# Kernel optimization log

Measured on AMD Instinct MI355X. Metric: run time of the kernel, lower is better.

Reference implementation:

```python
import jax, jax.numpy as jnp
import numpy as np

E = 256  # embedding_dim
H = 256  # hidden_dim
B = 65536


def setup_inputs() -> dict:
    key = jax.random.key(0)
    ks = jax.random.split(key, 15)
    inp = {
        "x": jax.random.normal(ks[0], (B, E), dtype=jnp.float32),
        "c": jax.random.normal(ks[1], (B, H), dtype=jnp.float32),
        "h": jax.random.normal(ks[2], (B, H), dtype=jnp.float32),
    }
    names = ["W_i", "U_i", "b_i", "W_f", "U_f", "b_f", "W_c", "U_c", "b_c", "W_o", "U_o", "b_o"]
    shapes = [(E, H), (H, H), (H,)] * 4
    for n, s, k in zip(names, shapes, ks[3:]):
        inp[n] = jax.random.normal(k, s, dtype=jnp.float32)
    return inp


def reference(x, c, h, W_i, U_i, b_i, W_f, U_f, b_f, W_c, U_c, b_c, W_o, U_o, b_o):
    # Batch the four input/hidden projections into two GEMMs, then fuse gates.
    W = jnp.concatenate([W_f, W_i, W_o, W_c], axis=1)  # [E, 4H]
    U = jnp.concatenate([U_f, U_i, U_o, U_c], axis=1)  # [H, 4H]
    b = jnp.concatenate([b_f, b_i, b_o, b_c], axis=0)  # [4H]
    z = x @ W + h @ U + b                               # [B, 4H]
    zf, zi, zo, zg = jnp.split(z, 4, axis=1)
    f = jax.nn.sigmoid(zf)
    i = jax.nn.sigmoid(zi)
    o = jax.nn.sigmoid(zo)
    g = jnp.tanh(zg)
    c_new = c * f + g * i
    h_new = o * jnp.tanh(c_new)
    return (c_new, h_new)
```

## Files before the change

kernel.cpp:

```cpp
#include <hip/hip_runtime.h>
#include <hip/hip_fp16.h>

typedef _Float16 half8 __attribute__((ext_vector_type(8)));
typedef _Float16 half4 __attribute__((ext_vector_type(4)));
typedef float f32x4 __attribute__((ext_vector_type(4)));

#define BHSZ 16777216
#define SLOT_BYTES 32768
#define B_OFF 16384
#define SBAR() __builtin_amdgcn_s_barrier()
#define WAITL() asm volatile("s_waitcnt lgkmcnt(0)" ::: "memory")

__device__ __forceinline__ void gload16(const void* g, const void* lds) {
  __builtin_amdgcn_global_load_lds((const __attribute__((address_space(1))) void*)g,
                                   (__attribute__((address_space(3))) void*)lds,
                                   16, 0, 0);
}

__device__ __forceinline__ float fast_sigmoid(float z) {
  float e = __builtin_amdgcn_exp2f(-z * 1.4426950408889634f);
  return __builtin_amdgcn_rcpf(1.0f + e);
}

__device__ __forceinline__ float fast_tanh(float z) {
  float a = __builtin_fabsf(z);
  float e = __builtin_amdgcn_exp2f(a * 2.8853900817779268f);
  float t = 1.0f - 2.0f * __builtin_amdgcn_rcpf(1.0f + e);
  return z < 0.0f ? -t : t;
}

__global__ __launch_bounds__(256) void pack_b(
    const float* __restrict__ Wf, const float* __restrict__ Uf,
    const float* __restrict__ Wi, const float* __restrict__ Ui,
    const float* __restrict__ Wo, const float* __restrict__ Uo,
    const float* __restrict__ Wc, const float* __restrict__ Uc,
    _Float16* __restrict__ Bp) {
  int idx = blockIdx.x * 256 + threadIdx.x;
  int k = idx & 511;
  int Np = idx >> 9;
  int g = (Np >> 4) & 3;
  int cl = ((Np >> 6) << 4) | (Np & 15);
  const float* W;
  const float* U;
  switch (g) {
    case 0: W = Wf; U = Uf; break;
    case 1: W = Wi; U = Ui; break;
    case 2: W = Wo; U = Uo; break;
    default: W = Wc; U = Uc; break;
  }
  float v = (k < 256) ? W[k * 256 + cl] : U[(k - 256) * 256 + cl];
  Bp[idx] = (_Float16)v;
}

__global__ __launch_bounds__(512, 2) void lstm_fused(
    const float* __restrict__ x, const float* __restrict__ h,
    const _Float16* __restrict__ Bp, const float* __restrict__ cin,
    const float* __restrict__ bf_, const float* __restrict__ bi_,
    const float* __restrict__ bo_, const float* __restrict__ bc_,
    float* __restrict__ out) {
  extern __shared__ __align__(16) char smem[];

  int tid = threadIdx.x;
  int w = tid >> 6, l = tid & 63;
  int l15 = l & 15, lg = l >> 4;
  int wr = w >> 2, wcn = w & 3;

  int bid = blockIdx.x;
  int wg = (bid & 7) * 128 + (bid >> 3);
  int bm = wg >> 2, bn = wg & 3;

  int aRowLo = tid >> 3;
  int aKpos = (tid & 7) * 4;
  int aWoff[4];
#pragma unroll
  for (int p = 0; p < 4; ++p) {
    int row = p * 64 + aRowLo;
    int rp = row >> 1;
    int c = ((((row & 1) << 2) | (aKpos >> 3)) ^ (rp & 7));
    aWoff[p] = rp * 128 + (c << 4) + ((tid & 1) << 3);
  }

  int fB[2];
#pragma unroll
  for (int p = 0; p < 2; ++p) {
    int d = p * 512 + tid;
    int rp = d >> 3, s8 = d & 7;
    int i8 = s8 ^ (rp & 7);
    int r = rp * 2 + (i8 >> 2), cb = i8 & 3;
    fB[p] = (bn * 256 + r) * 512 + (cb << 3);
  }
  int ldsB[2];
#pragma unroll
  for (int p = 0; p < 2; ++p) ldsB[p] = B_OFF + (p * 512 + w * 64) * 16;

  int offA[8], offB[4];
#pragma unroll
  for (int mf = 0; mf < 8; ++mf) {
    int r = wr * 128 + mf * 16 + l15;
    int rp = r >> 1;
    offA[mf] = rp * 128 + (((((r & 1) << 2) | lg) ^ (rp & 7)) << 4);
  }
#pragma unroll
  for (int nf = 0; nf < 4; ++nf) {
    int r = wcn * 64 + nf * 16 + l15;
    int rp = r >> 1;
    offB[nf] = B_OFF + rp * 128 + (((((r & 1) << 2) | lg) ^ (rp & 7)) << 4);
  }

  f32x4 acc[8][4];
#pragma unroll
  for (int a2 = 0; a2 < 8; ++a2)
#pragma unroll
    for (int b2 = 0; b2 < 4; ++b2)
      acc[a2][b2] = (f32x4){0.f, 0.f, 0.f, 0.f};

  f32x4 aReg[4];

  auto issueA = [&](int t) {
    const float* src = (t < 8) ? x : h;
    int kb = (t & 7) * 32;
#pragma unroll
    for (int p = 0; p < 4; ++p) {
      long row = (long)(bm * 256 + p * 64 + aRowLo);
      aReg[p] = *reinterpret_cast<const f32x4*>(src + row * 256 + kb + aKpos);
    }
  };
  auto issueB = [&](int t) {
    char* db = smem + (t % 3) * SLOT_BYTES;
#pragma unroll
    for (int p = 0; p < 2; ++p)
      gload16(Bp + fB[p] + t * 32, db + ldsB[p]);
  };
  auto writeA = [&](int t) {
    char* db = smem + (t % 3) * SLOT_BYTES;
#pragma unroll
    for (int p = 0; p < 4; ++p) {
      half4 o;
      o[0] = (_Float16)aReg[p][0]; o[1] = (_Float16)aReg[p][1];
      o[2] = (_Float16)aReg[p][2]; o[3] = (_Float16)aReg[p][3];
      *reinterpret_cast<half4*>(db + aWoff[p]) = o;
    }
  };

  issueB(0);
  issueA(0);
  asm volatile("s_waitcnt vmcnt(0)" ::: "memory");
  writeA(0);
  issueA(1);
  issueB(1);

#pragma unroll
  for (int j = 0; j < 16; ++j) {
    if (j == 15)
      asm volatile("s_waitcnt vmcnt(0)" ::: "memory");
    else
      asm volatile("s_waitcnt vmcnt(2)" ::: "memory");
    WAITL();
    SBAR();
    if (j <= 14) writeA(j + 1);
    if (j <= 13) issueA(j + 2);
    if (j <= 13) issueB(j + 2);

    const char* sb = smem + (j % 3) * SLOT_BYTES;
    half8 bv[4];
#pragma unroll
    for (int nf = 0; nf < 4; ++nf)
      bv[nf] = *reinterpret_cast<const half8*>(sb + offB[nf]);
#pragma unroll
    for (int bat = 0; bat < 2; ++bat) {
      half8 av[4];
#pragma unroll
      for (int q = 0; q < 4; ++q)
        av[q] = *reinterpret_cast<const half8*>(sb + offA[bat * 4 + q]);
      __builtin_amdgcn_s_setprio(1);
#pragma unroll
      for (int q = 0; q < 4; ++q)
#pragma unroll
        for (int nf = 0; nf < 4; ++nf)
          acc[bat * 4 + q][nf] = __builtin_amdgcn_mfma_f32_16x16x32_f16(
              av[q], bv[nf], acc[bat * 4 + q][nf], 0, 0, 0);
      __builtin_amdgcn_s_setprio(0);
    }
  }

  int col = (bn * 4 + wcn) * 16 + l15;
  float vbf = bf_[col], vbi = bi_[col], vbo = bo_[col], vbc = bc_[col];
#pragma unroll
  for (int mf = 0; mf < 8; ++mf) {
#pragma unroll
    for (int r = 0; r < 4; ++r) {
      long row = (long)(bm * 256 + wr * 128 + mf * 16 + lg * 4 + r);
      float zf = acc[mf][0][r] + vbf;
      float zi = acc[mf][1][r] + vbi;
      float zo = acc[mf][2][r] + vbo;
      float zg = acc[mf][3][r] + vbc;
      float fg = fast_sigmoid(zf);
      float ig = fast_sigmoid(zi);
      float og = fast_sigmoid(zo);
      float gg = fast_tanh(zg);
      float cv = cin[row * 256 + col];
      float cn = cv * fg + gg * ig;
      float hn = og * fast_tanh(cn);
      out[row * 256 + col] = cn;
      out[BHSZ + row * 256 + col] = hn;
    }
  }
}

extern "C" void kernel_launch(void* const* d_in, const int* in_sizes, int n_in,
                              void* d_out, int out_size, void* d_ws, size_t ws_size,
                              hipStream_t stream) {
  const float* x  = (const float*)d_in[0];
  const float* c  = (const float*)d_in[1];
  const float* h  = (const float*)d_in[2];
  const float* Wi = (const float*)d_in[3];
  const float* Ui = (const float*)d_in[4];
  const float* bi = (const float*)d_in[5];
  const float* Wf = (const float*)d_in[6];
  const float* Uf = (const float*)d_in[7];
  const float* bf = (const float*)d_in[8];
  const float* Wc = (const float*)d_in[9];
  const float* Uc = (const float*)d_in[10];
  const float* bc = (const float*)d_in[11];
  const float* Wo = (const float*)d_in[12];
  const float* Uo = (const float*)d_in[13];
  const float* bo = (const float*)d_in[14];

  _Float16* Bp = (_Float16*)d_ws;

  pack_b<<<2048, 256, 0, stream>>>(Wf, Uf, Wi, Ui, Wo, Uo, Wc, Uc, Bp);
  lstm_fused<<<1024, 512, 3 * SLOT_BYTES, stream>>>(x, h, Bp, c, bf, bi, bo,
                                                    bc, (float*)d_out);
}
```

Measured before the change: 149.1 us.

## Halve M-tile to 128 rows with 4 waves, double-buffer A, triple-buffer B

The workgroup tile drops from 256x256 to 128x256, run by 4 waves instead of 8 and launched as 2048 blocks. A is now double-buffered separately from triple-buffered B in a static 64KB LDS, and A stores are widened to 16-byte half8 writes. Sched barriers are added to pin the instruction order. Each B tile is now loaded by twice as many blocks, which raises L2 traffic for B, and with 64KB of LDS per block occupancy may fall.

```diff
diff --git a/kernel.cpp b/kernel.cpp
--- a/kernel.cpp
+++ b/kernel.cpp
@@ -2,13 +2,14 @@
 #include <hip/hip_fp16.h>
 
 typedef _Float16 half8 __attribute__((ext_vector_type(8)));
-typedef _Float16 half4 __attribute__((ext_vector_type(4)));
 typedef float f32x4 __attribute__((ext_vector_type(4)));
 
 #define BHSZ 16777216
-#define SLOT_BYTES 32768
-#define B_OFF 16384
+#define A_SLOT 8192
+#define B_SLOT 16384
+#define B_BASE 16384
 #define SBAR() __builtin_amdgcn_s_barrier()
+#define SCHEDB() __builtin_amdgcn_sched_barrier(0)
 #define WAITL() asm volatile("s_waitcnt lgkmcnt(0)" ::: "memory")
 
 __device__ __forceinline__ void gload16(const void* g, const void* lds) {
@@ -52,59 +53,56 @@
   Bp[idx] = (_Float16)v;
 }
 
-__global__ __launch_bounds__(512, 2) void lstm_fused(
+__global__ __launch_bounds__(256, 2) void lstm_fused(
     const float* __restrict__ x, const float* __restrict__ h,
     const _Float16* __restrict__ Bp, const float* __restrict__ cin,
     const float* __restrict__ bf_, const float* __restrict__ bi_,
     const float* __restrict__ bo_, const float* __restrict__ bc_,
     float* __restrict__ out) {
-  extern __shared__ __align__(16) char smem[];
+  __shared__ __align__(16) char smem[65536];
 
   int tid = threadIdx.x;
   int w = tid >> 6, l = tid & 63;
   int l15 = l & 15, lg = l >> 4;
-  int wr = w >> 2, wcn = w & 3;
 
   int bid = blockIdx.x;
-  int wg = (bid & 7) * 128 + (bid >> 3);
+  int wg = (bid & 7) * 256 + (bid >> 3);
   int bm = wg >> 2, bn = wg & 3;
 
-  int aRowLo = tid >> 3;
-  int aKpos = (tid & 7) * 4;
-  int aWoff[4];
+  int arow = tid >> 1;
+  int akq = (tid & 1) << 4;
+  const float* aSrcX = x + (long)(bm * 128 + arow) * 256 + akq;
+  const float* aSrcH = h + (long)(bm * 128 + arow) * 256 + akq;
+  int arp = arow >> 1;
+  int ac0 = ((arow & 1) << 2) | ((tid & 1) << 1);
+  int aW0 = arp * 128 + (((ac0 + 0) ^ (arp & 7)) << 4);
+  int aW1 = arp * 128 + (((ac0 + 1) ^ (arp & 7)) << 4);
+
+  int fB[4];
 #pragma unroll
   for (int p = 0; p < 4; ++p) {
-    int row = p * 64 + aRowLo;
-    int rp = row >> 1;
-    int c = ((((row & 1) << 2) | (aKpos >> 3)) ^ (rp & 7));
-    aWoff[p] = rp * 128 + (c << 4) + ((tid & 1) << 3);
-  }
-
-  int fB[2];
-#pragma unroll
-  for (int p = 0; p < 2; ++p) {
-    int d = p * 512 + tid;
+    int d = p * 256 + tid;
     int rp = d >> 3, s8 = d & 7;
     int i8 = s8 ^ (rp & 7);
     int r = rp * 2 + (i8 >> 2), cb = i8 & 3;
     fB[p] = (bn * 256 + r) * 512 + (cb << 3);
   }
-  int ldsB[2];
-#pragma unroll
-  for (int p = 0; p < 2; ++p) ldsB[p] = B_OFF + (p * 512 + w * 64) * 16;
+  int ldsB[4];
+#pragma unroll
+  for (int p = 0; p < 4; ++p) ldsB[p] = (p * 256 + w * 64) * 16;
 
   int offA[8], offB[4];
 #pragma unroll
   for (int mf = 0; mf < 8; ++mf) {
-    int r = wr * 128 + mf * 16 + l15;
+    int r = mf * 16 + l15;
     int rp = r >> 1;
     offA[mf] = rp * 128 + (((((r & 1) << 2) | lg) ^ (rp & 7)) << 4);
   }
 #pragma unroll
   for (int nf = 0; nf < 4; ++nf) {
-    int r = wcn * 64 + nf * 16 + l15;
+    int r = w * 64 + nf * 16 + l15;
     int rp = r >> 1;
-    offB[nf] = B_OFF + rp * 128 + (((((r & 1) << 2) | lg) ^ (rp & 7)) << 4);
+    offB[nf] = rp * 128 + (((((r & 1) << 2) | lg) ^ (rp & 7)) << 4);
   }
 
   f32x4 acc[8][4];
@@ -117,29 +115,30 @@
   f32x4 aReg[4];
 
   auto issueA = [&](int t) {
-    const float* src = (t < 8) ? x : h;
-    int kb = (t & 7) * 32;
-#pragma unroll
-    for (int p = 0; p < 4; ++p) {
-      long row = (long)(bm * 256 + p * 64 + aRowLo);
-      aReg[p] = *reinterpret_cast<const f32x4*>(src + row * 256 + kb + aKpos);
-    }
+    const float* src = ((t < 8) ? aSrcX : aSrcH) + (t & 7) * 32;
+#pragma unroll
+    for (int p = 0; p < 4; ++p)
+      aReg[p] = *reinterpret_cast<const f32x4*>(src + p * 4);
   };
   auto issueB = [&](int t) {
-    char* db = smem + (t % 3) * SLOT_BYTES;
-#pragma unroll
-    for (int p = 0; p < 2; ++p)
+    char* db = smem + B_BASE + (t % 3) * B_SLOT;
+#pragma unroll
+    for (int p = 0; p < 4; ++p)
       gload16(Bp + fB[p] + t * 32, db + ldsB[p]);
   };
   auto writeA = [&](int t) {
-    char* db = smem + (t % 3) * SLOT_BYTES;
-#pragma unroll
-    for (int p = 0; p < 4; ++p) {
-      half4 o;
-      o[0] = (_Float16)aReg[p][0]; o[1] = (_Float16)aReg[p][1];
-      o[2] = (_Float16)aReg[p][2]; o[3] = (_Float16)aReg[p][3];
-      *reinterpret_cast<half4*>(db + aWoff[p]) = o;
-    }
+    char* db = smem + (t & 1) * A_SLOT;
+    half8 h0, h1;
+    h0[0] = (_Float16)aReg[0][0]; h0[1] = (_Float16)aReg[0][1];
+    h0[2] = (_Float16)aReg[0][2]; h0[3] = (_Float16)aReg[0][3];
+    h0[4] = (_Float16)aReg[1][0]; h0[5] = (_Float16)aReg[1][1];
+    h0[6] = (_Float16)aReg[1][2]; h0[7] = (_Float16)aReg[1][3];
+    h1[0] = (_Float16)aReg[2][0]; h1[1] = (_Float16)aReg[2][1];
+    h1[2] = (_Float16)aReg[2][2]; h1[3] = (_Float16)aReg[2][3];
+    h1[4] = (_Float16)aReg[3][0]; h1[5] = (_Float16)aReg[3][1];
+    h1[6] = (_Float16)aReg[3][2]; h1[7] = (_Float16)aReg[3][3];
+    *reinterpret_cast<half8*>(db + aW0) = h0;
+    *reinterpret_cast<half8*>(db + aW1) = h1;
   };
 
   issueB(0);
@@ -154,14 +153,18 @@
     if (j == 15)
       asm volatile("s_waitcnt vmcnt(0)" ::: "memory");
     else
-      asm volatile("s_waitcnt vmcnt(2)" ::: "memory");
+      asm volatile("s_waitcnt vmcnt(4)" ::: "memory");
     WAITL();
     SBAR();
+    SCHEDB();
     if (j <= 14) writeA(j + 1);
-    if (j <= 13) issueA(j + 2);
-    if (j <= 13) issueB(j + 2);
-
-    const char* sb = smem + (j % 3) * SLOT_BYTES;
+    if (j <= 13) {
+      issueA(j + 2);
+      issueB(j + 2);
+    }
+
+    const char* sa = smem + (j & 1) * A_SLOT;
+    const char* sb = smem + B_BASE + (j % 3) * B_SLOT;
     half8 bv[4];
 #pragma unroll
     for (int nf = 0; nf < 4; ++nf)
@@ -171,7 +174,7 @@
       half8 av[4];
 #pragma unroll
       for (int q = 0; q < 4; ++q)
-        av[q] = *reinterpret_cast<const half8*>(sb + offA[bat * 4 + q]);
+        av[q] = *reinterpret_cast<const half8*>(sa + offA[bat * 4 + q]);
       __builtin_amdgcn_s_setprio(1);
 #pragma unroll
       for (int q = 0; q < 4; ++q)
@@ -181,15 +184,16 @@
               av[q], bv[nf], acc[bat * 4 + q][nf], 0, 0, 0);
       __builtin_amdgcn_s_setprio(0);
     }
-  }
-
-  int col = (bn * 4 + wcn) * 16 + l15;
+    SCHEDB();
+  }
+
+  int col = (bn * 4 + w) * 16 + l15;
   float vbf = bf_[col], vbi = bi_[col], vbo = bo_[col], vbc = bc_[col];
 #pragma unroll
   for (int mf = 0; mf < 8; ++mf) {
 #pragma unroll
     for (int r = 0; r < 4; ++r) {
-      long row = (long)(bm * 256 + wr * 128 + mf * 16 + lg * 4 + r);
+      long row = (long)(bm * 128 + mf * 16 + lg * 4 + r);
       float zf = acc[mf][0][r] + vbf;
       float zi = acc[mf][1][r] + vbi;
       float zo = acc[mf][2][r] + vbo;
@@ -229,6 +233,6 @@
   _Float16* Bp = (_Float16*)d_ws;
 
   pack_b<<<2048, 256, 0, stream>>>(Wf, Uf, Wi, Ui, Wo, Uo, Wc, Uc, Bp);
-  lstm_fused<<<1024, 512, 3 * SLOT_BYTES, stream>>>(x, h, Bp, c, bf, bi, bo,
-                                                    bc, (float*)d_out);
-}
+  lstm_fused<<<2048, 256, 0, stream>>>(x, h, Bp, c, bf, bi, bo, bc,
+                                       (float*)d_out);
+}
```

Measured after the change: 144.6 us. 3.1% less time.
